# Performance work log

Hardware: AMD Instinct MI355X
Metric: run time of the kernel (lower is better)

Reference implementation:

```python
import jax, jax.numpy as jnp
import numpy as np

NTOKEN = 50000
NINP = 256
NHID = 256
SEQ = 128
BSZ = 64
NS = 32
TEMP = 65.0
BIAS_REG = 1.0


def setup_inputs() -> dict:
    key = jax.random.key(0)
    ks = jax.random.split(key, 9)
    data = jax.random.randint(ks[0], (SEQ, BSZ), 0, NTOKEN)
    samples = jax.random.randint(ks[1], (NS, SEQ * BSZ), 0, NTOKEN)
    hidden = jax.random.normal(ks[2], (1, BSZ, NHID), dtype=jnp.float32) * 0.05
    emb_table = jax.random.uniform(ks[3], (NTOKEN, NINP), dtype=jnp.float32,
                                   minval=-0.1, maxval=0.1)  # matches init_weights uniform_(-0.1, 0.1)
    W_ih = jax.random.normal(ks[4], (NHID, NINP), dtype=jnp.float32) * 0.05
    b_ih = jax.random.normal(ks[5], (NHID,), dtype=jnp.float32) * 0.05
    W_hh = jax.random.normal(ks[6], (NHID, NHID), dtype=jnp.float32) * 0.05
    b_hh = jax.random.normal(ks[7], (NHID,), dtype=jnp.float32) * 0.05
    bias_vec = jax.random.normal(ks[8], (NTOKEN,), dtype=jnp.float32) * 0.05
    return dict(data=data, hidden=hidden, samples=samples, emb_table=emb_table,
                W_ih=W_ih, b_ih=b_ih, W_hh=W_hh, b_hh=b_hh, bias_vec=bias_vec)


def _eucl_dist(x, y, bias):
    # eucl distance score: negative squared euclidean distance plus per-token bias
    d = -jnp.sum((x - y) ** 2, axis=-1)
    return d + bias


def reference(data, hidden, samples, emb_table, W_ih, b_ih, W_hh, b_hh, bias_vec):
    S, B = data.shape
    emb = emb_table[data]  # (S, B, ninp); dropouts are 0 in eval mode

    def step(h, x_t):  # single-layer tanh RNN cell
        h_new = jnp.tanh(x_t @ W_ih.T + b_ih + h @ W_hh.T + b_hh)
        return h_new, h_new

    _, hs = jax.lax.scan(step, hidden[0], emb)        # (S, B, nhid)
    ro = jnp.concatenate([hidden, hs], axis=0)        # (S+1, B, nhid)

    # positive-sample distances: dist(h_{t-1}, h_t, bias[data_t])
    pos = _eucl_dist(ro[:-1], ro[1:], bias_vec[data])  # (S, B)
    x0 = (TEMP * pos).reshape(S * B)

    new_hidden = ro[-1][None]                          # (1, B, nhid)
    h_prev = ro[:-1].reshape(S * B, -1)                # (S*B, nhid)

    hU = h_prev @ W_hh.T + b_hh                        # (S*B, nhid)
    sW = jnp.einsum('npi,hi->nph', emb_table[samples], W_ih) + b_ih  # (NS, S*B, nhid)
    out = jnp.tanh(sW + hU[None])                      # vectorized over all negatives
    dneg = _eucl_dist(h_prev[None], out, bias_vec[samples])  # (NS, S*B)

    x = jnp.concatenate([x0[None], TEMP * dneg], axis=0)     # (1+NS, S*B)
    # logsoftmax activation: NCE-style loss, positives in row 0
    loss = jnp.mean(-jax.nn.log_softmax(x, axis=0)[0])
    loss = loss + BIAS_REG * jnp.sum(bias_vec ** 2)
    return loss, new_hidden
```

## Files before the change

### kernel.cpp

```cpp
#include <hip/hip_runtime.h>
#include <hip/hip_bf16.h>
#include <math.h>

#define SEQ   128
#define BSZ   64
#define NH    256
#define NT    50000
#define NSAMP 32
#define SB    8192
#define TEMPC 65.0f

typedef float f32x2 __attribute__((ext_vector_type(2)));

__device__ __forceinline__ float rlf(float v, int lane) {
  return __uint_as_float(__builtin_amdgcn_readlane(__float_as_uint(v), lane));
}

__device__ __forceinline__ float tanh_fast(float x) {
  float e = __expf(2.0f * x);
  return 1.0f - 2.0f * __builtin_amdgcn_rcpf(e + 1.0f);
}

__global__ void k_prep(const float* __restrict__ W_ih, float* __restrict__ Wt) {
  const int k = blockIdx.x, j = threadIdx.x;
  Wt[k * 256 + j] = W_ih[j * 256 + k];
}

__global__ __launch_bounds__(512, 4) void k_proj(const float* __restrict__ A,
    const float* __restrict__ Wt, const float* __restrict__ bias,
    float* __restrict__ out, int M) {
  __shared__ float As[64 * 257];
  const int t = threadIdx.x;
  const int l = t & 63;
  const int w = t >> 6;
  const int r0 = blockIdx.x * 64;

#pragma unroll
  for (int s = 0; s < 8; ++s) {
    int lin = t + s * 512;
    int row = lin >> 6, kq = lin & 63;
    float4 v = make_float4(0.f, 0.f, 0.f, 0.f);
    if (r0 + row < M) v = ((const float4*)A)[(size_t)(r0 + row) * 64 + kq];
    float* d = &As[row * 257 + kq * 4];
    d[0] = v.x; d[1] = v.y; d[2] = v.z; d[3] = v.w;
  }
  __syncthreads();

  const int c0 = w * 32;
  const float* wbase = Wt + __builtin_amdgcn_readfirstlane(c0);
  f32x2 acc2[16];
#pragma unroll
  for (int c = 0; c < 16; ++c) acc2[c] = (f32x2){0.f, 0.f};

#pragma unroll 2
  for (int kk = 0; kk < 256; ++kk) {
    float a = As[l * 257 + kk];
    f32x2 a2 = {a, a};
    const float4* wp = (const float4*)(wbase + (kk << 8));
#pragma unroll
    for (int c4 = 0; c4 < 8; ++c4) {
      float4 wv = wp[c4];
      f32x2 lo = {wv.x, wv.y}, hi = {wv.z, wv.w};
      acc2[2 * c4]     = __builtin_elementwise_fma(a2, lo, acc2[2 * c4]);
      acc2[2 * c4 + 1] = __builtin_elementwise_fma(a2, hi, acc2[2 * c4 + 1]);
    }
  }
  __syncthreads();

#pragma unroll
  for (int c = 0; c < 16; ++c) {
    As[l * 257 + c0 + 2 * c]     = acc2[c].x;
    As[l * 257 + c0 + 2 * c + 1] = acc2[c].y;
  }
  __syncthreads();
#pragma unroll
  for (int s = 0; s < 32; ++s) {
    int lin = t + s * 512;
    int row = lin >> 8, col = lin & 255;
    if (r0 + row < M)
      out[(size_t)(r0 + row) * 256 + col] = As[row * 257 + col] + bias[col];
  }
}

__global__ __launch_bounds__(512, 2) void k_scan(const float* __restrict__ proj,
    const int* __restrict__ data, const float* __restrict__ W_hh,
    const float* __restrict__ b_hh, const float* __restrict__ hidden,
    float* __restrict__ ro, float* __restrict__ hU, float* __restrict__ out) {
  __shared__ float part[2][8][256];
  __shared__ int   ldata[128];
  const int t = threadIdx.x, b = blockIdx.x;
  const int l = t & 63, w = t >> 6, w32 = w * 32;
  const int jv = w32 + (l & 31);

  f32x2 w01[32], w23[32];
  {
    const float4* r0 = (const float4*)(W_hh + (size_t)(l)*256 + w32);
    const float4* r1 = (const float4*)(W_hh + (size_t)(l + 64) * 256 + w32);
    const float4* r2 = (const float4*)(W_hh + (size_t)(l + 128) * 256 + w32);
    const float4* r3 = (const float4*)(W_hh + (size_t)(l + 192) * 256 + w32);
#pragma unroll
    for (int i4 = 0; i4 < 8; ++i4) {
      float4 v0 = r0[i4], v1 = r1[i4], v2 = r2[i4], v3 = r3[i4];
      w01[4 * i4 + 0] = (f32x2){v0.x, v1.x}; w01[4 * i4 + 1] = (f32x2){v0.y, v1.y};
      w01[4 * i4 + 2] = (f32x2){v0.z, v1.z}; w01[4 * i4 + 3] = (f32x2){v0.w, v1.w};
      w23[4 * i4 + 0] = (f32x2){v2.x, v3.x}; w23[4 * i4 + 1] = (f32x2){v2.y, v3.y};
      w23[4 * i4 + 2] = (f32x2){v2.z, v3.z}; w23[4 * i4 + 3] = (f32x2){v2.w, v3.w};
    }
  }
  if (t < 128) ldata[t] = data[t * 64 + b];
  __syncthreads();

  float hv = hidden[b * 256 + jv];
  if (l < 32) ro[b * 256 + jv] = hv;
  const float bhh = b_hh[jv];
  float xv = proj[(size_t)ldata[0] * 256 + jv];

  for (int st = 0; st < 128; ++st) {
    const int buf = st & 1;
    f32x2 a01a = {0.f, 0.f}, a01b = {0.f, 0.f};
    f32x2 a23a = {0.f, 0.f}, a23b = {0.f, 0.f};
#pragma unroll
    for (int i = 0; i < 32; i += 2) {
      float h0 = rlf(hv, i), h1 = rlf(hv, i + 1);
      f32x2 h0p = {h0, h0}, h1p = {h1, h1};
      a01a = __builtin_elementwise_fma(h0p, w01[i],     a01a);
      a23a = __builtin_elementwise_fma(h0p, w23[i],     a23a);
      a01b = __builtin_elementwise_fma(h1p, w01[i + 1], a01b);
      a23b = __builtin_elementwise_fma(h1p, w23[i + 1], a23b);
    }
    f32x2 a01 = a01a + a01b, a23 = a23a + a23b;
    part[buf][w][l]       = a01.x;
    part[buf][w][l + 64]  = a01.y;
    part[buf][w][l + 128] = a23.x;
    part[buf][w][l + 192] = a23.y;

    float xvn = 0.f;
    if (st < 127) xvn = proj[(size_t)ldata[st + 1] * 256 + jv];

    __syncthreads();

    float hu = ((part[buf][0][jv] + part[buf][1][jv])
              + (part[buf][2][jv] + part[buf][3][jv]))
             + ((part[buf][4][jv] + part[buf][5][jv])
              + (part[buf][6][jv] + part[buf][7][jv])) + bhh;
    float hn = tanh_fast(hu + xv);
    hv = hn;
    const int p = st * 64 + b;
    if (l < 32) {
      hU[(size_t)p * 256 + jv] = hu;
      ro[((size_t)p + 64) * 256 + jv] = hn;
      if (st == 127) out[1 + b * 256 + jv] = hn;
    }
    xv = xvn;
  }
}

__global__ __launch_bounds__(256, 4) void k_loss(const float* __restrict__ ro,
    const float* __restrict__ hU, const float* __restrict__ proj,
    const int* __restrict__ samples, const float* __restrict__ bias_vec,
    const int* __restrict__ data, float* __restrict__ lossP) {
  const int t = threadIdx.x, l = t & 63, w = t >> 6;
  const int p = blockIdx.x * 4 + w;
  float hp[4], hu[4];
  float x0v;
  {
    float dsq = 0.f;
#pragma unroll
    for (int q = 0; q < 4; ++q) {
      hp[q] = ro[(size_t)p * 256 + 64 * q + l];
      hu[q] = hU[(size_t)p * 256 + 64 * q + l];
      float hn = ro[((size_t)p + 64) * 256 + 64 * q + l];
      float d = hp[q] - hn;
      dsq = fmaf(d, d, dsq);
    }
#pragma unroll
    for (int m = 1; m < 64; m <<= 1) dsq += __shfl_xor(dsq, m);
    x0v = TEMPC * (bias_vec[data[p]] - dsq);
  }
  int   stok  = (l < 32) ? samples[(size_t)l * SB + p] : 0;
  float sbias = (l < 32) ? bias_vec[stok] : 0.f;

  float cr[4][4];
#pragma unroll
  for (int m = 0; m < 4; ++m) {
    int tk = __builtin_amdgcn_readlane(stok, m);
    const float* pr = proj + (size_t)tk * 256;
#pragma unroll
    for (int q = 0; q < 4; ++q) cr[m][q] = pr[64 * q + l];
  }

  float lg = 0.f;
  for (int n0 = 0; n0 < 32; n0 += 4) {
    float nx[4][4];
    if (n0 < 28) {
#pragma unroll
      for (int m = 0; m < 4; ++m) {
        int tk = __builtin_amdgcn_readlane(stok, n0 + 4 + m);
        const float* pr = proj + (size_t)tk * 256;
#pragma unroll
        for (int q = 0; q < 4; ++q) nx[m][q] = pr[64 * q + l];
      }
    }
    float s[4];
#pragma unroll
    for (int m = 0; m < 4; ++m) {
      float acc = 0.f;
#pragma unroll
      for (int q = 0; q < 4; ++q) {
        float o = tanh_fast(cr[m][q] + hu[q]);
        float d = hp[q] - o;
        acc = fmaf(d, d, acc);
      }
      s[m] = acc;
    }
#pragma unroll
    for (int sh = 1; sh < 64; sh <<= 1) {
#pragma unroll
      for (int m = 0; m < 4; ++m) s[m] += __shfl_xor(s[m], sh);
    }
#pragma unroll
    for (int m = 0; m < 4; ++m) {
      float bn = rlf(sbias, n0 + m);
      float logit = TEMPC * (bn - s[m]);
      if (l == n0 + m) lg = logit;
    }
    if (n0 < 28) {
#pragma unroll
      for (int m = 0; m < 4; ++m)
#pragma unroll
        for (int q = 0; q < 4; ++q) cr[m][q] = nx[m][q];
    }
  }

  float v = (l < 32) ? lg : ((l == 32) ? x0v : -INFINITY);
  float mx = v;
#pragma unroll
  for (int m = 1; m < 64; m <<= 1) mx = fmaxf(mx, __shfl_xor(mx, m));
  float e = (l < 33) ? __expf(v - mx) : 0.f;
#pragma unroll
  for (int m = 1; m < 64; m <<= 1) e += __shfl_xor(e, m);
  float lse = mx + __logf(e);

  __shared__ float bl[4];
  if (l == 0) bl[w] = lse - x0v;
  __syncthreads();
  if (t == 0) lossP[blockIdx.x] = (bl[0] + bl[1] + bl[2] + bl[3]);
}

__global__ __launch_bounds__(1024) void k_final(const float* __restrict__ lossP,
    const float* __restrict__ bv, float* __restrict__ out) {
  const int t = threadIdx.x, l = t & 63, w = t >> 6;
  float sa = 0.f;
  for (int i = t; i < 2048; i += 1024) sa += lossP[i];
  float sb = 0.f;
  for (int i = t; i < 12500; i += 1024) {
    float4 v = ((const float4*)bv)[i];
    sb += v.x * v.x + v.y * v.y + v.z * v.z + v.w * v.w;
  }
#pragma unroll
  for (int m = 1; m < 64; m <<= 1) {
    sa += __shfl_xor(sa, m);
    sb += __shfl_xor(sb, m);
  }
  __shared__ float wa[16], wb[16];
  if (l == 0) { wa[w] = sa; wb[w] = sb; }
  __syncthreads();
  if (t == 0) {
    float ta = 0.f, tb = 0.f;
#pragma unroll
    for (int i = 0; i < 16; ++i) { ta += wa[i]; tb += wb[i]; }
    out[0] = ta * (1.0f / 8192.0f) + tb;
  }
}

extern "C" void kernel_launch(void* const* d_in, const int* in_sizes, int n_in,
                              void* d_out, int out_size, void* d_ws, size_t ws_size,
                              hipStream_t stream) {
  const int*   data     = (const int*)  d_in[0];
  const float* hidden   = (const float*)d_in[1];
  const int*   samples  = (const int*)  d_in[2];
  const float* emb      = (const float*)d_in[3];
  const float* W_ih     = (const float*)d_in[4];
  const float* b_ih     = (const float*)d_in[5];
  const float* W_hh     = (const float*)d_in[6];
  const float* b_hh     = (const float*)d_in[7];
  const float* bias_vec = (const float*)d_in[8];
  float* out = (float*)d_out;
  float* ws  = (float*)d_ws;

  float* proj  = ws;
  float* Wt    = proj + 12800000;
  float* ro    = Wt + 65536;
  float* hU    = ro + 2113536;
  float* lossP = hU + 2097152;

  k_prep <<<256, 256, 0, stream>>>(W_ih, Wt);
  k_proj <<<782, 512, 0, stream>>>(emb, Wt, b_ih, proj, NT);
  k_scan <<<64, 512, 0, stream>>>(proj, data, W_hh, b_hh, hidden, ro, hU, out);
  k_loss <<<2048, 256, 0, stream>>>(ro, hU, proj, samples, bias_vec, data, lossP);
  k_final<<<1, 1024, 0, stream>>>(lossP, bias_vec, out);
}
```

Baseline: 355.7 us.

## Register-tile projection GEMM over 4x8 outputs and vectorize loss gathers to float4

```diff
diff --git a/kernel.cpp b/kernel.cpp
--- a/kernel.cpp
+++ b/kernel.cpp
@@ -31,8 +31,6 @@
     float* __restrict__ out, int M) {
   __shared__ float As[64 * 257];
   const int t = threadIdx.x;
-  const int l = t & 63;
-  const int w = t >> 6;
   const int r0 = blockIdx.x * 64;
 
 #pragma unroll
@@ -46,32 +44,44 @@
   }
   __syncthreads();
 
-  const int c0 = w * 32;
-  const float* wbase = Wt + __builtin_amdgcn_readfirstlane(c0);
-  f32x2 acc2[16];
-#pragma unroll
-  for (int c = 0; c < 16; ++c) acc2[c] = (f32x2){0.f, 0.f};
-
-#pragma unroll 2
-  for (int kk = 0; kk < 256; ++kk) {
-    float a = As[l * 257 + kk];
-    f32x2 a2 = {a, a};
-    const float4* wp = (const float4*)(wbase + (kk << 8));
-#pragma unroll
-    for (int c4 = 0; c4 < 8; ++c4) {
-      float4 wv = wp[c4];
-      f32x2 lo = {wv.x, wv.y}, hi = {wv.z, wv.w};
-      acc2[2 * c4]     = __builtin_elementwise_fma(a2, lo, acc2[2 * c4]);
-      acc2[2 * c4 + 1] = __builtin_elementwise_fma(a2, hi, acc2[2 * c4 + 1]);
-    }
-  }
-  __syncthreads();
-
-#pragma unroll
-  for (int c = 0; c < 16; ++c) {
-    As[l * 257 + c0 + 2 * c]     = acc2[c].x;
-    As[l * 257 + c0 + 2 * c + 1] = acc2[c].y;
-  }
+  const int rq = t & 15;
+  const int cg = t >> 4;
+  const float* wp = Wt + 8 * cg;
+
+  f32x2 acc[4][4];
+#pragma unroll
+  for (int m = 0; m < 4; ++m)
+#pragma unroll
+    for (int c = 0; c < 4; ++c) acc[m][c] = (f32x2){0.f, 0.f};
+
+  for (int kk = 0; kk < 256; kk += 2) {
+    const float4* wr0 = (const float4*)(wp + (kk << 8));
+    const float4* wr1 = (const float4*)(wp + ((kk + 1) << 8));
+    float4 wa0 = wr0[0], wa1 = wr0[1];
+    float4 wb0 = wr1[0], wb1 = wr1[1];
+    f32x2 wA[4] = {{wa0.x, wa0.y}, {wa0.z, wa0.w}, {wa1.x, wa1.y}, {wa1.z, wa1.w}};
+    f32x2 wB[4] = {{wb0.x, wb0.y}, {wb0.z, wb0.w}, {wb1.x, wb1.y}, {wb1.z, wb1.w}};
+#pragma unroll
+    for (int m = 0; m < 4; ++m) {
+      float a0 = As[(rq + 16 * m) * 257 + kk];
+      float a1 = As[(rq + 16 * m) * 257 + kk + 1];
+      f32x2 a0p = {a0, a0}, a1p = {a1, a1};
+#pragma unroll
+      for (int c = 0; c < 4; ++c) {
+        acc[m][c] = __builtin_elementwise_fma(a0p, wA[c], acc[m][c]);
+        acc[m][c] = __builtin_elementwise_fma(a1p, wB[c], acc[m][c]);
+      }
+    }
+  }
+  __syncthreads();
+
+#pragma unroll
+  for (int m = 0; m < 4; ++m)
+#pragma unroll
+    for (int c = 0; c < 4; ++c) {
+      As[(rq + 16 * m) * 257 + 8 * cg + 2 * c]     = acc[m][c].x;
+      As[(rq + 16 * m) * 257 + 8 * cg + 2 * c + 1] = acc[m][c].y;
+    }
   __syncthreads();
 #pragma unroll
   for (int s = 0; s < 32; ++s) {
@@ -161,18 +171,17 @@
     const int* __restrict__ data, float* __restrict__ lossP) {
   const int t = threadIdx.x, l = t & 63, w = t >> 6;
   const int p = blockIdx.x * 4 + w;
-  float hp[4], hu[4];
+  const float4 hp4 = ((const float4*)(ro + (size_t)p * 256))[l];
+  const float4 hn4 = ((const float4*)(ro + ((size_t)p + 64) * 256))[l];
+  const float4 hu4 = ((const float4*)(hU + (size_t)p * 256))[l];
   float x0v;
   {
-    float dsq = 0.f;
-#pragma unroll
-    for (int q = 0; q < 4; ++q) {
-      hp[q] = ro[(size_t)p * 256 + 64 * q + l];
-      hu[q] = hU[(size_t)p * 256 + 64 * q + l];
-      float hn = ro[((size_t)p + 64) * 256 + 64 * q + l];
-      float d = hp[q] - hn;
-      dsq = fmaf(d, d, dsq);
-    }
+    float dx = hp4.x - hn4.x, dy = hp4.y - hn4.y;
+    float dz = hp4.z - hn4.z, dw = hp4.w - hn4.w;
+    float dsq = dx * dx;
+    dsq = fmaf(dy, dy, dsq);
+    dsq = fmaf(dz, dz, dsq);
+    dsq = fmaf(dw, dw, dsq);
 #pragma unroll
     for (int m = 1; m < 64; m <<= 1) dsq += __shfl_xor(dsq, m);
     x0v = TEMPC * (bias_vec[data[p]] - dsq);
@@ -180,37 +189,35 @@
   int   stok  = (l < 32) ? samples[(size_t)l * SB + p] : 0;
   float sbias = (l < 32) ? bias_vec[stok] : 0.f;
 
-  float cr[4][4];
+  float4 cr[4];
 #pragma unroll
   for (int m = 0; m < 4; ++m) {
     int tk = __builtin_amdgcn_readlane(stok, m);
-    const float* pr = proj + (size_t)tk * 256;
-#pragma unroll
-    for (int q = 0; q < 4; ++q) cr[m][q] = pr[64 * q + l];
+    cr[m] = ((const float4*)(proj + (size_t)tk * 256))[l];
   }
 
   float lg = 0.f;
   for (int n0 = 0; n0 < 32; n0 += 4) {
-    float nx[4][4];
+    float4 nx[4];
     if (n0 < 28) {
 #pragma unroll
       for (int m = 0; m < 4; ++m) {
         int tk = __builtin_amdgcn_readlane(stok, n0 + 4 + m);
-        const float* pr = proj + (size_t)tk * 256;
-#pragma unroll
-        for (int q = 0; q < 4; ++q) nx[m][q] = pr[64 * q + l];
+        nx[m] = ((const float4*)(proj + (size_t)tk * 256))[l];
       }
     }
     float s[4];
 #pragma unroll
     for (int m = 0; m < 4; ++m) {
-      float acc = 0.f;
-#pragma unroll
-      for (int q = 0; q < 4; ++q) {
-        float o = tanh_fast(cr[m][q] + hu[q]);
-        float d = hp[q] - o;
-        acc = fmaf(d, d, acc);
-      }
+      float o0 = tanh_fast(cr[m].x + hu4.x);
+      float o1 = tanh_fast(cr[m].y + hu4.y);
+      float o2 = tanh_fast(cr[m].z + hu4.z);
+      float o3 = tanh_fast(cr[m].w + hu4.w);
+      float d0 = hp4.x - o0, d1 = hp4.y - o1, d2 = hp4.z - o2, d3 = hp4.w - o3;
+      float acc = d0 * d0;
+      acc = fmaf(d1, d1, acc);
+      acc = fmaf(d2, d2, acc);
+      acc = fmaf(d3, d3, acc);
       s[m] = acc;
     }
 #pragma unroll
@@ -226,9 +233,7 @@
     }
     if (n0 < 28) {
 #pragma unroll
-      for (int m = 0; m < 4; ++m)
-#pragma unroll
-        for (int q = 0; q < 4; ++q) cr[m][q] = nx[m][q];
+      for (int m = 0; m < 4; ++m) cr[m] = nx[m];
     }
   }
 
```

Measured after the change: 376.4 us. 5.8% more time.
